# Performance work log

Measured on AMD Instinct MI355X. Metric: run time of the kernel, lower is better.

Reference implementation:

```python
import jax, jax.numpy as jnp
import numpy as np

HEAD_DIM = 128
INFTY_APPROX = 1e+30
ROTARY_BASE = 10000.0

B, T, M = 2, 2048, 1024
H = M // HEAD_DIM  # 8


def setup_inputs() -> dict:
    key = jax.random.key(0)
    ks = jax.random.split(key, 5)
    x = jax.random.normal(ks[0], (B, T, M), dtype=jnp.float32)
    # mu-param inits: wq zeros in the original; use small random here for a
    # non-degenerate numerical baseline, scaled like kv_init = d_model**-0.5
    scale = M ** (-0.5)
    wq = jax.random.normal(ks[1], (M, H, HEAD_DIM), dtype=jnp.float32) * scale
    wk = jax.random.normal(ks[2], (M, H, HEAD_DIM), dtype=jnp.float32) * scale
    wv = jax.random.normal(ks[3], (M, H, HEAD_DIM), dtype=jnp.float32) * scale
    wo = jax.random.normal(ks[4], (H, HEAD_DIM, M), dtype=jnp.float32) * scale
    return {"x": x, "wq": wq, "wk": wk, "wv": wv, "wo": wo}


def _rotary(x, base=ROTARY_BASE):
    # x: [..., T, W]; non-interpretable RoPE over even/odd halves of W
    length, width = x.shape[-2], x.shape[-1]
    half = width // 2
    positions = jnp.arange(length)[:, None].astype(x.dtype)          # [T,1]
    ang_freqs = jnp.power(base, -jnp.arange(half) / half)[None, :]   # [1,half]
    radians = positions * ang_freqs                                  # [T,half]
    cos = jnp.cos(radians).astype(x.dtype)
    sin = jnp.sin(radians).astype(x.dtype)
    even, odd = jnp.split(x, 2, axis=-1)
    return jnp.concatenate([even * cos - odd * sin,
                            even * sin + odd * cos], axis=-1)


def _fractional_rotary(x):
    # rotary on first half of head dim, passthrough on the rest
    rot, skip = jnp.split(x, 2, axis=-1)
    return jnp.concatenate([_rotary(rot), skip], axis=-1)


def reference(x, wq, wk, wv, wo):
    q = jnp.einsum('bim,mhd->bhid', x, wq)
    k = jnp.einsum('bim,mhd->bhid', x, wk)
    v = jnp.einsum('bim,mhd->bhid', x, wv)
    q = _fractional_rotary(q)
    k = _fractional_rotary(k)
    # mu-param attention: scale by 1/HEAD_DIM (not 1/sqrt(D))
    s = jnp.einsum('bhid,bhjd->bhij', q, k) / HEAD_DIM
    i = jnp.arange(T)[:, None]
    j = jnp.arange(T)[None, :]
    mask = (i < j).astype(s.dtype)  # strictly-upper-triangular
    s = s - jnp.asarray(INFTY_APPROX, dtype=s.dtype) * mask
    p = jax.nn.softmax(s, axis=-1)
    o = jnp.einsum('bhij,bhjd->bhid', p, v)
    r = jnp.einsum('bhid,hdm->bim', o, wo)
    return r
```

## Files before the change

kernel.cpp:

```cpp
#include <hip/hip_runtime.h>

#define T_SEQ 2048
#define MDL   1024
#define NH    8
#define HD    128

typedef __bf16 bf16;
typedef __bf16 bf16x8 __attribute__((ext_vector_type(8)));
typedef __bf16 bf16x4 __attribute__((ext_vector_type(4)));
typedef float  f32x4  __attribute__((ext_vector_type(4)));

#define GLB(p) ((const __attribute__((address_space(1))) void*)(p))
#define LDS(p) ((__attribute__((address_space(3))) void*)(p))

#if __has_builtin(__builtin_amdgcn_exp2f)
#define EXP2(x) __builtin_amdgcn_exp2f(x)
#else
#define EXP2(x) __expf((x) * 0.6931471805599453f)
#endif

#define QSCALE 0.011271055f


__global__ __launch_bounds__(256) void prep_kernel(
    const float* __restrict__ x,
    const float* __restrict__ wq, const float* __restrict__ wk,
    const float* __restrict__ wv, const float* __restrict__ wo,
    bf16* __restrict__ xb, bf16* __restrict__ Wt, bf16* __restrict__ Wot)
{
    __shared__ bf16 t_lds[64 * 72];
    const int tid = threadIdx.x;
    if (blockIdx.x < 2048) {
        size_t i = ((size_t)blockIdx.x * 256 + tid) * 8;
        float4 v0 = *(const float4*)(x + i);
        float4 v1 = *(const float4*)(x + i + 4);
        bf16x8 o;
        o[0]=(bf16)v0.x; o[1]=(bf16)v0.y; o[2]=(bf16)v0.z; o[3]=(bf16)v0.w;
        o[4]=(bf16)v1.x; o[5]=(bf16)v1.y; o[6]=(bf16)v1.z; o[7]=(bf16)v1.w;
        *(bf16x8*)(xb + i) = o;
        return;
    }
    const int bx = blockIdx.x - 2048;
    const int sec = bx >> 8;
    const int tile = bx & 255;
    const int k0 = (tile >> 4) * 64, n0 = (tile & 15) * 64;
    const float* src = sec == 0 ? wq : sec == 1 ? wk : sec == 2 ? wv : wo;
    bf16* dst = sec < 3 ? (Wt + (size_t)sec * MDL * MDL) : Wot;

    const int ir = tid >> 2, jc = (tid & 3) * 16;
    const float* sp = src + (size_t)(k0 + ir) * MDL + n0 + jc;
    #pragma unroll
    for (int c = 0; c < 4; ++c) {
        float4 v = *(const float4*)(sp + c * 4);
        bf16x4 o; o[0]=(bf16)v.x; o[1]=(bf16)v.y; o[2]=(bf16)v.z; o[3]=(bf16)v.w;
        *(bf16x4*)&t_lds[ir * 72 + jc + c * 4] = o;
    }
    __syncthreads();
    bf16x8 o0, o1;
    #pragma unroll
    for (int jj = 0; jj < 8; ++jj) {
        o0[jj] = t_lds[(jc + jj) * 72 + ir];
        o1[jj] = t_lds[(jc + 8 + jj) * 72 + ir];
    }
    bf16* dp = dst + (size_t)(n0 + ir) * MDL + k0 + jc;
    *(bf16x8*)dp = o0;
    *(bf16x8*)(dp + 8) = o1;
}

__global__ __launch_bounds__(256) void qkv_rope_kernel(
    const bf16* __restrict__ xb, const bf16* __restrict__ Wt,
    bf16* __restrict__ Qb, bf16* __restrict__ Kt, bf16* __restrict__ Vt)
{
    __shared__ bf16 smem[8192];
    bf16* a_lds = smem;
    bf16* b_lds = smem + 4096;

    const int tid = threadIdx.x, bx = blockIdx.x;
    const int nt = bx % 24, mt = bx / 24;
    const int n0 = nt * 128, m0 = mt * 128;
    const int section = n0 >> 10;
    const int h = (n0 & 1023) >> 7;

    const int lane = tid & 63, w = tid >> 6;
    const int quad = lane >> 4, l15 = lane & 15;
    const int wr = w >> 1, wc = w & 1;
    const int lrow = lane >> 2, lsub = lane & 3;

    const bf16* gA = xb + (size_t)m0 * MDL + lsub * 8;
    const bf16* gB = Wt + (size_t)n0 * MDL + lsub * 8;

    f32x4 acc[4][4] = {};

    for (int k0 = 0; k0 < MDL; k0 += 32) {
        #pragma unroll
        for (int i = 0; i < 2; ++i) {
            const int ch = w * 2 + i;
            const int row = ch * 16 + lrow;
            __builtin_amdgcn_global_load_lds(GLB(gA + (size_t)row * MDL + k0),
                                             LDS(&a_lds[ch * 16 * 32]), 16, 0, 0);
            __builtin_amdgcn_global_load_lds(GLB(gB + (size_t)row * MDL + k0),
                                             LDS(&b_lds[ch * 16 * 32]), 16, 0, 0);
        }
        __syncthreads();

        bf16x8 af[4], bfr[4];
        #pragma unroll
        for (int mi = 0; mi < 4; ++mi)
            af[mi] = *(const bf16x8*)&a_lds[(wr * 64 + mi * 16 + l15) * 32 + quad * 8];
        #pragma unroll
        for (int ni = 0; ni < 4; ++ni)
            bfr[ni] = *(const bf16x8*)&b_lds[(wc * 64 + ni * 16 + l15) * 32 + quad * 8];
        #pragma unroll
        for (int mi = 0; mi < 4; ++mi)
            #pragma unroll
            for (int ni = 0; ni < 4; ++ni)
                acc[mi][ni] = __builtin_amdgcn_mfma_f32_16x16x32_bf16(af[mi], bfr[ni], acc[mi][ni], 0, 0, 0);
        __syncthreads();
    }

    const int bdx = m0 >> 11;
    const int t0 = m0 & (T_SEQ - 1);
    const int bh = bdx * NH + h;

    if (section == 2) {
        #pragma unroll
        for (int c = 0; c < 2; ++c) {
            if (wc == c) {
                #pragma unroll
                for (int mi = 0; mi < 4; ++mi)
                    #pragma unroll
                    for (int r = 0; r < 4; ++r) {
                        int p = 16 * quad + 4 * r + mi;
                        int base = (wr * 8 + (p >> 3)) * 512 + (p & 7);
                        #pragma unroll
                        for (int ni = 0; ni < 4; ++ni)
                            smem[base + (ni * 16 + l15) * 8] = (bf16)acc[mi][ni][r];
                    }
            }
            __syncthreads();
            {
                const int t8 = tid >> 4;
                bf16* vp = Vt + ((size_t)(bh * 32 + (t0 >> 6) + (t8 >> 3))) * 8192
                              + (t8 & 7) * 1024 + c * 512 + (tid & 15) * 32;
                #pragma unroll
                for (int k = 0; k < 4; ++k)
                    *(bf16x8*)(vp + k * 8) = *(const bf16x8*)&smem[tid * 32 + k * 8];
            }
            __syncthreads();
        }
        return;
    }

    float fr_n[2];
    #pragma unroll
    for (int ni = 0; ni < 2; ++ni)
        fr_n[ni] = __expf(-(float)(ni * 16 + l15) * 0.28782313662425573f);

    if (section == 0) {
        #pragma unroll
        for (int mi = 0; mi < 4; ++mi) {
            #pragma unroll
            for (int r = 0; r < 4; ++r) {
                int t = t0 + wr * 64 + mi * 16 + quad * 4 + r;
                bf16* orow = Qb + ((size_t)bh * T_SEQ + t) * HD;
                if (wc == 0) {
                    #pragma unroll
                    for (int ni = 0; ni < 2; ++ni) {
                        int d = ni * 16 + l15;
                        float ang = (float)t * fr_n[ni];
                        float sn = __sinf(ang), cs = __cosf(ang);
                        float ev = acc[mi][ni][r];
                        float ov = acc[mi][ni + 2][r];
                        orow[d]      = (bf16)((ev * cs - ov * sn) * QSCALE);
                        orow[d + 32] = (bf16)((ev * sn + ov * cs) * QSCALE);
                    }
                } else {
                    #pragma unroll
                    for (int ni = 0; ni < 4; ++ni)
                        orow[64 + ni * 16 + l15] = (bf16)(acc[mi][ni][r] * QSCALE);
                }
            }
        }
    } else {
        #pragma unroll
        for (int c = 0; c < 2; ++c) {
            if (wr == c) {
                #pragma unroll
                for (int mi = 0; mi < 4; ++mi) {
                    #pragma unroll
                    for (int r = 0; r < 4; ++r) {
                        int tl = mi * 16 + quad * 4 + r;
                        int t = t0 + c * 64 + tl;
                        if (wc == 0) {
                            #pragma unroll
                            for (int ni = 0; ni < 2; ++ni) {
                                int d = ni * 16 + l15;
                                float ang = (float)t * fr_n[ni];
                                float sn = __sinf(ang), cs = __cosf(ang);
                                float ev = acc[mi][ni][r];
                                float ov = acc[mi][ni + 2][r];
                                smem[(d >> 3) * 512 + tl * 8 + (d & 7)] = (bf16)(ev * cs - ov * sn);
                                int d2 = d + 32;
                                smem[(d2 >> 3) * 512 + tl * 8 + (d2 & 7)] = (bf16)(ev * sn + ov * cs);
                            }
                        } else {
                            #pragma unroll
                            for (int ni = 0; ni < 4; ++ni) {
                                int d = 64 + ni * 16 + l15;
                                smem[(d >> 3) * 512 + tl * 8 + (d & 7)] = (bf16)acc[mi][ni][r];
                            }
                        }
                    }
                }
            }
            __syncthreads();
            {
                bf16* kp = Kt + ((size_t)(bh * 32 + (t0 >> 6) + c)) * 8192 + tid * 32;
                #pragma unroll
                for (int k = 0; k < 4; ++k)
                    *(bf16x8*)(kp + k * 8) = *(const bf16x8*)&smem[tid * 32 + k * 8];
            }
            __syncthreads();
        }
    }
}

template <int SP>
__global__ __launch_bounds__(256) void attn_kernel(
    const bf16* __restrict__ Qb, const bf16* __restrict__ Kt,
    const bf16* __restrict__ Vt, bf16* __restrict__ PO, float* __restrict__ Pl)
{
    __shared__ bf16 k_lds[8192];
    __shared__ bf16 v_lds[8192];
    __shared__ bf16 p_lds[4][32 * 72];

    const int tid = threadIdx.x, lane = tid & 63, w = tid >> 6;
    const int quad = lane >> 4, l15 = lane & 15;
    const int bx = blockIdx.x;
    const int s0 = bx % SP;
    const int ip = (bx / SP) & 7;
    const int bh = bx / (SP * 8);
    const int tA = 2 * ip + 2;

    const bf16* Kbh = Kt + (size_t)bh * 32 * 8192;
    const bf16* Vbh = Vt + (size_t)bh * 32 * 8192;

    bf16x8 kreg[4], vreg[4];
    bf16x8 qf[2][4];
    f32x4 Of[2][8];
    float l_r[2][4];

    auto fetch = [&](int g) {
        const int jt = (g < tA) ? g : g - tA;
        const bf16* kt = Kbh + (size_t)jt * 8192 + tid * 8;
        const bf16* vt = Vbh + (size_t)jt * 8192 + tid * 8;
        #pragma unroll
        for (int k = 0; k < 4; ++k) {
            kreg[k] = *(const bf16x8*)(kt + k * 2048);
            vreg[k] = *(const bf16x8*)(vt + k * 2048);
        }
    };

    fetch(s0);
    int pqt = -1;

    #pragma unroll 1
    for (int g = s0; g < 34; g += SP) {
        const int ph = (g >= tA);
        const int qt = ph ? 15 - ip : ip;
        const int jt = ph ? g - tA : g;

        if (qt != pqt) {
            if (pqt >= 0) {
                const size_t slot = ((size_t)bh * 16 + pqt) * SP + s0;
                #pragma unroll
                for (int mi = 0; mi < 2; ++mi)
                    #pragma unroll
                    for (int r = 0; r < 4; ++r) {
                        float ls = l_r[mi][r];
                        ls += __shfl_xor(ls, 1); ls += __shfl_xor(ls, 2);
                        ls += __shfl_xor(ls, 4); ls += __shfl_xor(ls, 8);
                        const int row = w * 32 + mi * 16 + quad * 4 + r;
                        if (l15 == 0) Pl[slot * 128 + row] = ls;
                        bf16* pr = PO + (slot * 128 + row) * 128;
                        #pragma unroll
                        for (int di = 0; di < 8; ++di)
                            pr[di * 16 + l15] = (bf16)Of[mi][di][r];
                    }
            }
            #pragma unroll
            for (int mi = 0; mi < 2; ++mi) {
                const bf16* qrow = Qb + ((size_t)bh * T_SEQ + qt * 128 + w * 32 + mi * 16 + l15) * HD + quad * 8;
                #pragma unroll
                for (int kk = 0; kk < 4; ++kk)
                    qf[mi][kk] = *(const bf16x8*)(qrow + kk * 32);
                #pragma unroll
                for (int di = 0; di < 8; ++di) Of[mi][di] = (f32x4){0.f, 0.f, 0.f, 0.f};
                #pragma unroll
                for (int r = 0; r < 4; ++r) l_r[mi][r] = 0.f;
            }
            pqt = qt;
        }

        __syncthreads();
        #pragma unroll
        for (int k = 0; k < 4; ++k) {
            *(bf16x8*)&k_lds[k * 2048 + tid * 8] = kreg[k];
            *(bf16x8*)&v_lds[k * 2048 + tid * 8] = vreg[k];
        }
        if (g + SP < 34) fetch(g + SP);
        __syncthreads();

        f32x4 sa[2][4] = {};
        #pragma unroll
        for (int kk = 0; kk < 4; ++kk) {
            bf16x8 kb[4];
            #pragma unroll
            for (int ni = 0; ni < 4; ++ni)
                kb[ni] = *(const bf16x8*)&k_lds[(kk * 4 + quad) * 512 + (ni * 16 + l15) * 8];
            #pragma unroll
            for (int ni = 0; ni < 4; ++ni)
                #pragma unroll
                for (int mi = 0; mi < 2; ++mi)
                    sa[mi][ni] = __builtin_amdgcn_mfma_f32_16x16x32_bf16(qf[mi][kk], kb[ni], sa[mi][ni], 0, 0, 0);
        }

        const bool diag = (jt >= 2 * qt);
        #pragma unroll
        for (int mi = 0; mi < 2; ++mi) {
            const int rowb = w * 32 + mi * 16 + quad * 4;
            #pragma unroll
            for (int r = 0; r < 4; ++r) {
                float ps = 0.f;
                bf16x4 pq;
                #pragma unroll
                for (int ni = 0; ni < 4; ++ni) {
                    float pv = EXP2(sa[mi][ni][r]);
                    if (diag && (jt * 64 + ni * 16 + l15) > (qt * 128 + rowb + r)) pv = 0.f;
                    ps += pv;
                    pq[ni] = (bf16)pv;
                }
                *(bf16x4*)&p_lds[w][(mi * 16 + quad * 4 + r) * 72 + l15 * 4] = pq;
                l_r[mi][r] += ps;
            }
        }

        #pragma unroll
        for (int kk = 0; kk < 2; ++kk) {
            bf16x8 pa[2];
            #pragma unroll
            for (int mi = 0; mi < 2; ++mi)
                pa[mi] = *(const bf16x8*)&p_lds[w][(mi * 16 + l15) * 72 + kk * 32 + quad * 8];
            #pragma unroll
            for (int di = 0; di < 8; ++di) {
                bf16x8 vb = *(const bf16x8*)&v_lds[(kk * 4 + quad) * 1024 + (di * 16 + l15) * 8];
                #pragma unroll
                for (int mi = 0; mi < 2; ++mi)
                    Of[mi][di] = __builtin_amdgcn_mfma_f32_16x16x32_bf16(pa[mi], vb, Of[mi][di], 0, 0, 0);
            }
        }
    }

    {
        const size_t slot = ((size_t)bh * 16 + pqt) * SP + s0;
        #pragma unroll
        for (int mi = 0; mi < 2; ++mi)
            #pragma unroll
            for (int r = 0; r < 4; ++r) {
                float ls = l_r[mi][r];
                ls += __shfl_xor(ls, 1); ls += __shfl_xor(ls, 2);
                ls += __shfl_xor(ls, 4); ls += __shfl_xor(ls, 8);
                const int row = w * 32 + mi * 16 + quad * 4 + r;
                if (l15 == 0) Pl[slot * 128 + row] = ls;
                bf16* pr = PO + (slot * 128 + row) * 128;
                #pragma unroll
                for (int di = 0; di < 8; ++di)
                    pr[di * 16 + l15] = (bf16)Of[mi][di][r];
            }
    }
}

template <int SP>
__global__ __launch_bounds__(256) void attn_combine_kernel(
    const bf16* __restrict__ PO, const float* __restrict__ Pl,
    bf16* __restrict__ Ob)
{
    const int idx = blockIdx.x * 256 + threadIdx.x;
    const int dcol = (idx & 15) * 8;
    const int rowg = idx >> 4;
    const int bh = rowg >> 11, qrow = rowg & 2047;
    const int qt = qrow >> 7, row = qrow & 127;
    const int ns = (2 * qt + 2 < SP) ? (2 * qt + 2) : SP;

    float acc[8] = {};
    float l = 0.f;
    for (int s = 0; s < ns; ++s) {
        const size_t base = (((size_t)bh * 16 + qt) * SP + s) * 128 + row;
        bf16x8 po = *(const bf16x8*)&PO[base * 128 + dcol];
        #pragma unroll
        for (int jj = 0; jj < 8; ++jj) acc[jj] += (float)po[jj];
        l += Pl[base];
    }
    const float inv = 1.f / l;
    const int b = bh >> 3, hh = bh & 7, t = qt * 128 + row;
    bf16x8 o;
    #pragma unroll
    for (int jj = 0; jj < 8; ++jj) o[jj] = (bf16)(acc[jj] * inv);
    *(bf16x8*)(Ob + ((size_t)(b * T_SEQ + t) * NH + hh) * HD + dcol) = o;
}

__global__ __launch_bounds__(256) void out_proj_kernel(
    const bf16* __restrict__ Ob, const bf16* __restrict__ Wot,
    float* __restrict__ out)
{
    __shared__ bf16 a_lds[128 * 32];
    __shared__ bf16 b_lds[128 * 32];

    const int tid = threadIdx.x, bx = blockIdx.x;
    const int nt = bx & 7, mt = bx >> 3;
    const int n0 = nt * 128, m0 = mt * 128;

    const int lane = tid & 63, w = tid >> 6;
    const int quad = lane >> 4, l15 = lane & 15;
    const int wr = w >> 1, wc = w & 1;
    const int lrow = lane >> 2, lsub = lane & 3;

    const bf16* gA = Ob  + (size_t)m0 * MDL + lsub * 8;
    const bf16* gB = Wot + (size_t)n0 * MDL + lsub * 8;

    f32x4 acc[4][4] = {};

    for (int k0 = 0; k0 < MDL; k0 += 32) {
        #pragma unroll
        for (int i = 0; i < 2; ++i) {
            const int ch = w * 2 + i;
            const int row = ch * 16 + lrow;
            __builtin_amdgcn_global_load_lds(GLB(gA + (size_t)row * MDL + k0),
                                             LDS(&a_lds[ch * 16 * 32]), 16, 0, 0);
            __builtin_amdgcn_global_load_lds(GLB(gB + (size_t)row * MDL + k0),
                                             LDS(&b_lds[ch * 16 * 32]), 16, 0, 0);
        }
        __syncthreads();

        bf16x8 af[4], bfr[4];
        #pragma unroll
        for (int mi = 0; mi < 4; ++mi)
            af[mi] = *(const bf16x8*)&a_lds[(wr * 64 + mi * 16 + l15) * 32 + quad * 8];
        #pragma unroll
        for (int ni = 0; ni < 4; ++ni)
            bfr[ni] = *(const bf16x8*)&b_lds[(wc * 64 + ni * 16 + l15) * 32 + quad * 8];
        #pragma unroll
        for (int mi = 0; mi < 4; ++mi)
            #pragma unroll
            for (int ni = 0; ni < 4; ++ni)
                acc[mi][ni] = __builtin_amdgcn_mfma_f32_16x16x32_bf16(af[mi], bfr[ni], acc[mi][ni], 0, 0, 0);
        __syncthreads();
    }

    #pragma unroll
    for (int mi = 0; mi < 4; ++mi)
        #pragma unroll
        for (int r = 0; r < 4; ++r) {
            int row_g = m0 + wr * 64 + mi * 16 + quad * 4 + r;
            float* crow = out + (size_t)row_g * MDL + n0;
            #pragma unroll
            for (int ni = 0; ni < 4; ++ni)
                crow[wc * 64 + ni * 16 + l15] = acc[mi][ni][r];
        }
}

extern "C" void kernel_launch(void* const* d_in, const int* in_sizes, int n_in,
                              void* d_out, int out_size, void* d_ws, size_t ws_size,
                              hipStream_t stream) {
    const float* x  = (const float*)d_in[0];
    const float* wq = (const float*)d_in[1];
    const float* wk = (const float*)d_in[2];
    const float* wv = (const float*)d_in[3];
    const float* wo = (const float*)d_in[4];
    float* out = (float*)d_out;

    const size_t NTOK = (size_t)2 * NH * T_SEQ * HD;
    bf16*  Qb  = (bf16*)d_ws;
    bf16*  Kt  = Qb + NTOK;
    bf16*  Vt  = Kt + NTOK;
    bf16*  Ob  = Vt + NTOK;
    bf16*  Wot = Ob + NTOK;
    bf16*  PO  = Wot + (size_t)MDL * MDL;

    bf16* xbuf = (bf16*)d_out;
    bf16* Wt   = xbuf + (size_t)4096 * MDL;

    prep_kernel<<<3072, 256, 0, stream>>>(x, wq, wk, wv, wo, xbuf, Wt, Wot);
    qkv_rope_kernel<<<768, 256, 0, stream>>>(xbuf, Wt, Qb, Kt, Vt);

    const size_t fixed_b = ((size_t)NTOK * 4 + (size_t)MDL * MDL) * sizeof(bf16);
    const size_t need6 = fixed_b + (size_t)16 * 16 * 6 * 128 * 128 * sizeof(bf16)
                                 + (size_t)16 * 16 * 6 * 128 * sizeof(float);
    if (ws_size >= need6) {
        float* Pl = (float*)(PO + (size_t)16 * 16 * 6 * 128 * 128);
        attn_kernel<6><<<16 * 8 * 6, 256, 0, stream>>>(Qb, Kt, Vt, PO, Pl);
        attn_combine_kernel<6><<<2048, 256, 0, stream>>>(PO, Pl, Ob);
    } else {
        float* Pl = (float*)(PO + (size_t)16 * 16 * 4 * 128 * 128);
        attn_kernel<4><<<16 * 8 * 4, 256, 0, stream>>>(Qb, Kt, Vt, PO, Pl);
        attn_combine_kernel<4><<<2048, 256, 0, stream>>>(PO, Pl, Ob);
    }
    out_proj_kernel<<<256, 256, 0, stream>>>(Ob, Wot, out);
}
```

Measured before the change: 202.3 us.

## Load K/V tiles directly to LDS and remap blocks to XCDs by head

Replaces the register-staged K/V prefetch (global load into registers, then LDS store) with direct global-to-LDS loads issued at the start of each iteration. It also remaps block indices so that blocks on the same XCD share a batch-head and can reuse its K/V in L2, and it raises launch bounds to request 4 blocks per CU. The register prefetch is dropped, so loads are no longer overlapped with the previous tile's compute and each iteration stalls on the load before the barrier. In exchange, register pressure falls enough that higher occupancy may hide that latency.

```diff
diff --git a/kernel.cpp b/kernel.cpp
--- a/kernel.cpp
+++ b/kernel.cpp
@@ -226,7 +226,7 @@
 }
 
 template <int SP>
-__global__ __launch_bounds__(256) void attn_kernel(
+__global__ __launch_bounds__(256, 4) void attn_kernel(
     const bf16* __restrict__ Qb, const bf16* __restrict__ Kt,
     const bf16* __restrict__ Vt, bf16* __restrict__ PO, float* __restrict__ Pl)
 {
@@ -237,31 +237,34 @@
     const int tid = threadIdx.x, lane = tid & 63, w = tid >> 6;
     const int quad = lane >> 4, l15 = lane & 15;
     const int bx = blockIdx.x;
-    const int s0 = bx % SP;
-    const int ip = (bx / SP) & 7;
-    const int bh = bx / (SP * 8);
-    const int tA = 2 * ip + 2;
+    const int xcd  = bx & 7;
+    const int slot = bx >> 3;
+    const int bh   = xcd * 2 + (slot >= 8 * SP);
+    const int w2   = slot % (8 * SP);
+    const int ip   = w2 / SP;
+    const int s0   = w2 % SP;
+    const int tA   = 2 * ip + 2;
 
     const bf16* Kbh = Kt + (size_t)bh * 32 * 8192;
     const bf16* Vbh = Vt + (size_t)bh * 32 * 8192;
 
-    bf16x8 kreg[4], vreg[4];
     bf16x8 qf[2][4];
     f32x4 Of[2][8];
     float l_r[2][4];
 
-    auto fetch = [&](int g) {
+    auto stage = [&](int g) {
         const int jt = (g < tA) ? g : g - tA;
         const bf16* kt = Kbh + (size_t)jt * 8192 + tid * 8;
         const bf16* vt = Vbh + (size_t)jt * 8192 + tid * 8;
         #pragma unroll
         for (int k = 0; k < 4; ++k) {
-            kreg[k] = *(const bf16x8*)(kt + k * 2048);
-            vreg[k] = *(const bf16x8*)(vt + k * 2048);
+            __builtin_amdgcn_global_load_lds(GLB(kt + k * 2048),
+                                             LDS(&k_lds[k * 2048 + w * 512]), 16, 0, 0);
+            __builtin_amdgcn_global_load_lds(GLB(vt + k * 2048),
+                                             LDS(&v_lds[k * 2048 + w * 512]), 16, 0, 0);
         }
     };
 
-    fetch(s0);
     int pqt = -1;
 
     #pragma unroll 1
@@ -272,7 +275,7 @@
 
         if (qt != pqt) {
             if (pqt >= 0) {
-                const size_t slot = ((size_t)bh * 16 + pqt) * SP + s0;
+                const size_t slotq = ((size_t)bh * 16 + pqt) * SP + s0;
                 #pragma unroll
                 for (int mi = 0; mi < 2; ++mi)
                     #pragma unroll
@@ -281,8 +284,8 @@
                         ls += __shfl_xor(ls, 1); ls += __shfl_xor(ls, 2);
                         ls += __shfl_xor(ls, 4); ls += __shfl_xor(ls, 8);
                         const int row = w * 32 + mi * 16 + quad * 4 + r;
-                        if (l15 == 0) Pl[slot * 128 + row] = ls;
-                        bf16* pr = PO + (slot * 128 + row) * 128;
+                        if (l15 == 0) Pl[slotq * 128 + row] = ls;
+                        bf16* pr = PO + (slotq * 128 + row) * 128;
                         #pragma unroll
                         for (int di = 0; di < 8; ++di)
                             pr[di * 16 + l15] = (bf16)Of[mi][di][r];
@@ -303,12 +306,7 @@
         }
 
         __syncthreads();
-        #pragma unroll
-        for (int k = 0; k < 4; ++k) {
-            *(bf16x8*)&k_lds[k * 2048 + tid * 8] = kreg[k];
-            *(bf16x8*)&v_lds[k * 2048 + tid * 8] = vreg[k];
-        }
-        if (g + SP < 34) fetch(g + SP);
+        stage(g);
         __syncthreads();
 
         f32x4 sa[2][4] = {};
@@ -362,7 +360,7 @@
     }
 
     {
-        const size_t slot = ((size_t)bh * 16 + pqt) * SP + s0;
+        const size_t slotq = ((size_t)bh * 16 + pqt) * SP + s0;
         #pragma unroll
         for (int mi = 0; mi < 2; ++mi)
             #pragma unroll
@@ -371,8 +369,8 @@
                 ls += __shfl_xor(ls, 1); ls += __shfl_xor(ls, 2);
                 ls += __shfl_xor(ls, 4); ls += __shfl_xor(ls, 8);
                 const int row = w * 32 + mi * 16 + quad * 4 + r;
-                if (l15 == 0) Pl[slot * 128 + row] = ls;
-                bf16* pr = PO + (slot * 128 + row) * 128;
+                if (l15 == 0) Pl[slotq * 128 + row] = ls;
+                bf16* pr = PO + (slotq * 128 + row) * 128;
                 #pragma unroll
                 for (int di = 0; di < 8; ++di)
                     pr[di * 16 + l15] = (bf16)Of[mi][di][r];
```

Result: faster. 196.9 us (-2.7%).
